# Performance work log

Measured on AMD Instinct MI355X. Metric: run time of the kernel, lower is better.

## Reference

```python
import jax, jax.numpy as jnp
import numpy as np

MARGIN_NEG = 0.4
MARGIN_POS = 0.01


def setup_inputs() -> dict:
    key = jax.random.key(0)
    k1, k2, k3, k4, k5, k6 = jax.random.split(key, 6)
    B, C, H, W = 64, 3, 256, 256
    zc, zh, zw = 64, 16, 16
    return {
        "outputs1": jax.random.normal(k1, (B, C, H, W), dtype=jnp.float32),
        "z1": jax.random.uniform(k2, (B, zc, zh, zw), dtype=jnp.float32),
        "outputs2": jax.random.normal(k3, (B, C, H, W), dtype=jnp.float32),
        "z2": jax.random.uniform(k4, (B, zc, zh, zw), dtype=jnp.float32),
        "input1": jax.random.normal(k5, (B, C, H, W), dtype=jnp.float32),
        "input2": jax.random.normal(k6, (B, C, H, W), dtype=jnp.float32),
    }


def _contrastive_loss(z1, z2):
    # Faithful vectorization of the nested (m, n) loop in Contrastive_loss.
    B = z1.shape[0]
    z1f = z1.reshape(B, -1)  # [B, D]
    z2f = z2.reshape(B, -1)  # [B, D]
    D = z1f.shape[1]
    # Pairwise mean-squared distance via the matmul trick:
    # d[m, n] = mean((z1[m] - z2[n])**2)
    sq1 = jnp.sum(z1f * z1f, axis=1)  # [B]
    sq2 = jnp.sum(z2f * z2f, axis=1)  # [B]
    cross = z1f @ z2f.T               # [B, B]
    d = (sq1[:, None] + sq2[None, :] - 2.0 * cross) / D  # [B, B]

    eye = jnp.eye(B, dtype=bool)
    diag = jnp.diagonal(d)  # [B]
    # positive pairs (m == n): accumulate (d - margin_pos) where d > margin_pos
    lossP = jnp.sum(jnp.where(diag > MARGIN_POS, diag - MARGIN_POS, 0.0))
    # negative pairs (m != n): accumulate (margin_neg - d) where d < margin_neg
    neg = jnp.where((~eye) & (d < MARGIN_NEG), MARGIN_NEG - d, 0.0)
    lossN = jnp.sum(neg)

    lossP = lossP / B
    if B > 1:
        lossN = lossN / (B * (B - 1))
    return 1.5 * lossP + 0.5 * lossN


def reference(outputs1, z1, outputs2, z2, input1, input2):
    # MSE_and_Contrastive_loss with eps=1, useOnlyPair=False
    eps = 1.0
    recon = jnp.mean((outputs1 - input1) ** 2) + jnp.mean((outputs2 - input2) ** 2)
    sim = _contrastive_loss(z1, z2)
    return recon + eps * sim
```

## Files before the change

### kernel.cpp

```cpp
#include <hip/hip_runtime.h>

#define MARGIN_NEG 0.4f
#define MARGIN_POS 0.01f

#define N_ELEM   12582912
#define N4       (N_ELEM / 4)
#define BATCH    64
#define DIMZ     16384


__global__ void mse_kernel(const float4* __restrict__ o1, const float4* __restrict__ i1,
                           const float4* __restrict__ o2, const float4* __restrict__ i2,
                           double* __restrict__ ws) {
    int tid = blockIdx.x * blockDim.x + threadIdx.x;
    int stride = gridDim.x * blockDim.x;
    float acc = 0.f;
    for (int i = tid; i < N4; i += stride) {
        float4 a = o1[i], b = i1[i];
        float dx = a.x - b.x, dy = a.y - b.y, dz = a.z - b.z, dw = a.w - b.w;
        acc += dx * dx + dy * dy + dz * dz + dw * dw;
        float4 c = o2[i], d = i2[i];
        dx = c.x - d.x; dy = c.y - d.y; dz = c.z - d.z; dw = c.w - d.w;
        acc += dx * dx + dy * dy + dz * dz + dw * dw;
    }
    #pragma unroll
    for (int off = 32; off > 0; off >>= 1) acc += __shfl_down(acc, off, 64);
    __shared__ float warp_sums[4];
    int lane = threadIdx.x & 63, wid = threadIdx.x >> 6;
    if (lane == 0) warp_sums[wid] = acc;
    __syncthreads();
    if (threadIdx.x == 0) {
        float s = warp_sums[0] + warp_sums[1] + warp_sums[2] + warp_sums[3];
        atomicAdd(ws, (double)s);
    }
}

__global__ void contrastive_kernel(const float* __restrict__ z1, const float* __restrict__ z2,
                                   double* __restrict__ ws) {
    const int TM = 4, TN = 4;
    int m0 = (blockIdx.x >> 4) * TM;
    int n0 = (blockIdx.x & 15) * TN;
    int t = threadIdx.x;
    int lane = t & 63, wid = t >> 6;

    float acc[16];
    #pragma unroll
    for (int p = 0; p < 16; p++) acc[p] = 0.f;

    const float4* z1v = (const float4*)z1;
    const float4* z2v = (const float4*)z2;
    const int row4 = DIMZ / 4;
    for (int c = t; c < row4; c += 256) {
        float4 a[TM], b[TN];
        #pragma unroll
        for (int i = 0; i < TM; i++) a[i] = z1v[(m0 + i) * row4 + c];
        #pragma unroll
        for (int j = 0; j < TN; j++) b[j] = z2v[(n0 + j) * row4 + c];
        #pragma unroll
        for (int i = 0; i < TM; i++) {
            #pragma unroll
            for (int j = 0; j < TN; j++) {
                float dx = a[i].x - b[j].x, dy = a[i].y - b[j].y;
                float dz = a[i].z - b[j].z, dw = a[i].w - b[j].w;
                acc[i * TN + j] += dx * dx + dy * dy + dz * dz + dw * dw;
            }
        }
    }

    __shared__ float wsum[4][16];
    #pragma unroll
    for (int p = 0; p < 16; p++) {
        float v = acc[p];
        #pragma unroll
        for (int off = 32; off > 0; off >>= 1) v += __shfl_down(v, off, 64);
        if (lane == 0) wsum[wid][p] = v;
    }
    __syncthreads();

    if (t < 16) {
        float s = wsum[0][t] + wsum[1][t] + wsum[2][t] + wsum[3][t];
        float d = s * (1.0f / (float)DIMZ);
        int m = m0 + (t >> 2), n = n0 + (t & 3);
        float p = 0.f, q = 0.f;
        if (m == n) {
            if (d > MARGIN_POS) p = d - MARGIN_POS;
        } else {
            if (d < MARGIN_NEG) q = MARGIN_NEG - d;
        }
        #pragma unroll
        for (int off = 8; off > 0; off >>= 1) {
            p += __shfl_down(p, off, 64);
            q += __shfl_down(q, off, 64);
        }
        if (t == 0) {
            if (p != 0.f) atomicAdd(ws + 1, (double)p);
            if (q != 0.f) atomicAdd(ws + 2, (double)q);
        }
    }
}

__global__ void finalize_kernel(const double* __restrict__ ws, float* __restrict__ out) {
    double recon = ws[0] / (double)N_ELEM;
    double lossP = ws[1] / (double)BATCH;
    double lossN = ws[2] / ((double)BATCH * (double)(BATCH - 1));
    out[0] = (float)(recon + 1.5 * lossP + 0.5 * lossN);
}

extern "C" void kernel_launch(void* const* d_in, const int* in_sizes, int n_in,
                              void* d_out, int out_size, void* d_ws, size_t ws_size,
                              hipStream_t stream) {
    const float* outputs1 = (const float*)d_in[0];
    const float* z1       = (const float*)d_in[1];
    const float* outputs2 = (const float*)d_in[2];
    const float* z2       = (const float*)d_in[3];
    const float* input1   = (const float*)d_in[4];
    const float* input2   = (const float*)d_in[5];
    float* out = (float*)d_out;
    double* ws = (double*)d_ws;

    hipMemsetAsync(ws, 0, 3 * sizeof(double), stream);

    mse_kernel<<<2048, 256, 0, stream>>>((const float4*)outputs1, (const float4*)input1,
                                         (const float4*)outputs2, (const float4*)input2, ws);
    contrastive_kernel<<<256, 256, 0, stream>>>(z1, z2, ws);
    finalize_kernel<<<1, 1, 0, stream>>>(ws, out);
}
```

Before: 234.8 us.

## Fuse MSE and contrastive passes into one launch with split-K tiles

Merges the MSE reduction and the pairwise contrastive distance computation into a single kernel. Block ranges are split by role: 1024 blocks compute 4x4 distance tiles over quarter-K chunks and atomically add them into a float 64x64 matrix, and 4096 blocks each cover a fixed unrolled strip of one MSE pair. A 256-thread second kernel applies the margins and writes the final loss. This removes one launch, raises parallelism in the contrastive part, and replaces double atomics with float ones, at the cost of a larger memset and reduced summation precision.

```diff
diff --git a/kernel.cpp b/kernel.cpp
--- a/kernel.cpp
+++ b/kernel.cpp
@@ -7,103 +7,126 @@
 #define N4       (N_ELEM / 4)
 #define BATCH    64
 #define DIMZ     16384
+#define ROW4     (DIMZ / 4)
 
+#define CB   1024
+#define MBP  2048
+#define TPP  (MBP * 256)
+#define MSE_ITERS (N4 / TPP)
 
-__global__ void mse_kernel(const float4* __restrict__ o1, const float4* __restrict__ i1,
-                           const float4* __restrict__ o2, const float4* __restrict__ i2,
-                           double* __restrict__ ws) {
-    int tid = blockIdx.x * blockDim.x + threadIdx.x;
-    int stride = gridDim.x * blockDim.x;
-    float acc = 0.f;
-    for (int i = tid; i < N4; i += stride) {
-        float4 a = o1[i], b = i1[i];
-        float dx = a.x - b.x, dy = a.y - b.y, dz = a.z - b.z, dw = a.w - b.w;
-        acc += dx * dx + dy * dy + dz * dz + dw * dw;
-        float4 c = o2[i], d = i2[i];
-        dx = c.x - d.x; dy = c.y - d.y; dz = c.z - d.z; dw = c.w - d.w;
-        acc += dx * dx + dy * dy + dz * dz + dw * dw;
-    }
-    #pragma unroll
-    for (int off = 32; off > 0; off >>= 1) acc += __shfl_down(acc, off, 64);
-    __shared__ float warp_sums[4];
-    int lane = threadIdx.x & 63, wid = threadIdx.x >> 6;
-    if (lane == 0) warp_sums[wid] = acc;
-    __syncthreads();
-    if (threadIdx.x == 0) {
-        float s = warp_sums[0] + warp_sums[1] + warp_sums[2] + warp_sums[3];
-        atomicAdd(ws, (double)s);
+#define WS_MSE_IDX 4160
+#define WS_FLOATS  4161
+
+__global__ __launch_bounds__(256) void fused_pass1(
+        const float* __restrict__ o1, const float* __restrict__ i1,
+        const float* __restrict__ o2, const float* __restrict__ i2,
+        const float* __restrict__ z1, const float* __restrict__ z2,
+        float* __restrict__ ws) {
+    const int b = blockIdx.x;
+    const int t = threadIdx.x;
+    const int lane = t & 63, wid = t >> 6;
+
+    if (b < CB) {
+        const int kc   = b & 3;
+        const int tile = b >> 2;
+        const int m0 = (tile >> 4) * 4;
+        const int n0 = (tile & 15) * 4;
+        const float4* z1v = (const float4*)z1;
+        const float4* z2v = (const float4*)z2;
+
+        float acc[16];
+        #pragma unroll
+        for (int p = 0; p < 16; p++) acc[p] = 0.f;
+
+        const int cbase = kc * 1024 + t;
+        #pragma unroll
+        for (int it = 0; it < 4; it++) {
+            const int c = cbase + it * 256;
+            float4 a[4], bb[4];
+            #pragma unroll
+            for (int i = 0; i < 4; i++) a[i] = z1v[(m0 + i) * ROW4 + c];
+            #pragma unroll
+            for (int j = 0; j < 4; j++) bb[j] = z2v[(n0 + j) * ROW4 + c];
+            #pragma unroll
+            for (int i = 0; i < 4; i++) {
+                #pragma unroll
+                for (int j = 0; j < 4; j++) {
+                    float dx = a[i].x - bb[j].x, dy = a[i].y - bb[j].y;
+                    float dz = a[i].z - bb[j].z, dw = a[i].w - bb[j].w;
+                    acc[i * 4 + j] += dx * dx + dy * dy + dz * dz + dw * dw;
+                }
+            }
+        }
+
+        __shared__ float wsum[4][16];
+        #pragma unroll
+        for (int p = 0; p < 16; p++) {
+            float v = acc[p];
+            #pragma unroll
+            for (int off = 32; off > 0; off >>= 1) v += __shfl_down(v, off, 64);
+            if (lane == 0) wsum[wid][p] = v;
+        }
+        __syncthreads();
+        if (t < 16) {
+            float s = wsum[0][t] + wsum[1][t] + wsum[2][t] + wsum[3][t];
+            int m = m0 + (t >> 2), n = n0 + (t & 3);
+            atomicAdd(&ws[m * 64 + n], s);
+        }
+    } else {
+        int mb = b - CB;
+        const float4 *A, *Bv;
+        if (mb < MBP) { A = (const float4*)o1; Bv = (const float4*)i1; }
+        else          { A = (const float4*)o2; Bv = (const float4*)i2; mb -= MBP; }
+        const int tid = mb * 256 + t;
+
+        float acc0 = 0.f, acc1 = 0.f;
+        #pragma unroll
+        for (int s = 0; s < MSE_ITERS; s += 2) {
+            float4 x0 = A[tid + s * TPP],       y0 = Bv[tid + s * TPP];
+            float4 x1 = A[tid + (s + 1) * TPP], y1 = Bv[tid + (s + 1) * TPP];
+            float a0 = x0.x - y0.x, a1 = x0.y - y0.y, a2 = x0.z - y0.z, a3 = x0.w - y0.w;
+            acc0 += a0 * a0 + a1 * a1 + a2 * a2 + a3 * a3;
+            float b0 = x1.x - y1.x, b1 = x1.y - y1.y, b2 = x1.z - y1.z, b3 = x1.w - y1.w;
+            acc1 += b0 * b0 + b1 * b1 + b2 * b2 + b3 * b3;
+        }
+        float v = acc0 + acc1;
+        #pragma unroll
+        for (int off = 32; off > 0; off >>= 1) v += __shfl_down(v, off, 64);
+        __shared__ float ws4[4];
+        if (lane == 0) ws4[wid] = v;
+        __syncthreads();
+        if (t == 0) atomicAdd(&ws[WS_MSE_IDX], ws4[0] + ws4[1] + ws4[2] + ws4[3]);
     }
 }
 
-__global__ void contrastive_kernel(const float* __restrict__ z1, const float* __restrict__ z2,
-                                   double* __restrict__ ws) {
-    const int TM = 4, TN = 4;
-    int m0 = (blockIdx.x >> 4) * TM;
-    int n0 = (blockIdx.x & 15) * TN;
-    int t = threadIdx.x;
-    int lane = t & 63, wid = t >> 6;
-
-    float acc[16];
+__global__ __launch_bounds__(256) void fused_pass2(const float* __restrict__ ws,
+                                                   float* __restrict__ out) {
+    const int t = threadIdx.x;
+    const int lane = t & 63, wid = t >> 6;
+    float p = 0.f, q = 0.f;
     #pragma unroll
-    for (int p = 0; p < 16; p++) acc[p] = 0.f;
-
-    const float4* z1v = (const float4*)z1;
-    const float4* z2v = (const float4*)z2;
-    const int row4 = DIMZ / 4;
-    for (int c = t; c < row4; c += 256) {
-        float4 a[TM], b[TN];
-        #pragma unroll
-        for (int i = 0; i < TM; i++) a[i] = z1v[(m0 + i) * row4 + c];
-        #pragma unroll
-        for (int j = 0; j < TN; j++) b[j] = z2v[(n0 + j) * row4 + c];
-        #pragma unroll
-        for (int i = 0; i < TM; i++) {
-            #pragma unroll
-            for (int j = 0; j < TN; j++) {
-                float dx = a[i].x - b[j].x, dy = a[i].y - b[j].y;
-                float dz = a[i].z - b[j].z, dw = a[i].w - b[j].w;
-                acc[i * TN + j] += dx * dx + dy * dy + dz * dz + dw * dw;
-            }
-        }
+    for (int s = 0; s < 16; s++) {
+        int idx = t + s * 256;
+        float d = ws[idx] * (1.0f / (float)DIMZ);
+        int m = idx >> 6, n = idx & 63;
+        if (m == n) { if (d > MARGIN_POS) p += d - MARGIN_POS; }
+        else        { if (d < MARGIN_NEG) q += MARGIN_NEG - d; }
     }
-
-    __shared__ float wsum[4][16];
     #pragma unroll
-    for (int p = 0; p < 16; p++) {
-        float v = acc[p];
-        #pragma unroll
-        for (int off = 32; off > 0; off >>= 1) v += __shfl_down(v, off, 64);
-        if (lane == 0) wsum[wid][p] = v;
+    for (int off = 32; off > 0; off >>= 1) {
+        p += __shfl_down(p, off, 64);
+        q += __shfl_down(q, off, 64);
     }
+    __shared__ float sp[4], sq[4];
+    if (lane == 0) { sp[wid] = p; sq[wid] = q; }
     __syncthreads();
-
-    if (t < 16) {
-        float s = wsum[0][t] + wsum[1][t] + wsum[2][t] + wsum[3][t];
-        float d = s * (1.0f / (float)DIMZ);
-        int m = m0 + (t >> 2), n = n0 + (t & 3);
-        float p = 0.f, q = 0.f;
-        if (m == n) {
-            if (d > MARGIN_POS) p = d - MARGIN_POS;
-        } else {
-            if (d < MARGIN_NEG) q = MARGIN_NEG - d;
-        }
-        #pragma unroll
-        for (int off = 8; off > 0; off >>= 1) {
-            p += __shfl_down(p, off, 64);
-            q += __shfl_down(q, off, 64);
-        }
-        if (t == 0) {
-            if (p != 0.f) atomicAdd(ws + 1, (double)p);
-            if (q != 0.f) atomicAdd(ws + 2, (double)q);
-        }
+    if (t == 0) {
+        float P = sp[0] + sp[1] + sp[2] + sp[3];
+        float Q = sq[0] + sq[1] + sq[2] + sq[3];
+        float recon = ws[WS_MSE_IDX] * (1.0f / (float)N_ELEM);
+        out[0] = recon + 1.5f * (P / (float)BATCH)
+                       + 0.5f * (Q / (float)(BATCH * (BATCH - 1)));
     }
-}
-
-__global__ void finalize_kernel(const double* __restrict__ ws, float* __restrict__ out) {
-    double recon = ws[0] / (double)N_ELEM;
-    double lossP = ws[1] / (double)BATCH;
-    double lossN = ws[2] / ((double)BATCH * (double)(BATCH - 1));
-    out[0] = (float)(recon + 1.5 * lossP + 0.5 * lossN);
 }
 
 extern "C" void kernel_launch(void* const* d_in, const int* in_sizes, int n_in,
@@ -116,12 +139,11 @@
     const float* input1   = (const float*)d_in[4];
     const float* input2   = (const float*)d_in[5];
     float* out = (float*)d_out;
-    double* ws = (double*)d_ws;
+    float* ws  = (float*)d_ws;
 
-    hipMemsetAsync(ws, 0, 3 * sizeof(double), stream);
+    hipMemsetAsync(ws, 0, WS_FLOATS * sizeof(float), stream);
 
-    mse_kernel<<<2048, 256, 0, stream>>>((const float4*)outputs1, (const float4*)input1,
-                                         (const float4*)outputs2, (const float4*)input2, ws);
-    contrastive_kernel<<<256, 256, 0, stream>>>(z1, z2, ws);
-    finalize_kernel<<<1, 1, 0, stream>>>(ws, out);
+    fused_pass1<<<CB + 2 * MBP, 256, 0, stream>>>(outputs1, input1, outputs2, input2,
+                                                  z1, z2, ws);
+    fused_pass2<<<1, 256, 0, stream>>>(ws, out);
 }
```

Result: faster. 222.8 us (-5.1%).
